# Kernel optimization log

Measured on AMD Instinct MI355X. Metric: run time of the kernel, lower is better.

Reference implementation:

```python
import jax, jax.numpy as jnp
import numpy as np

NHEAD = 16


def setup_inputs() -> dict:
    key = jax.random.key(0)
    ks = jax.random.split(key, 6)
    S, B, D = 2048, 2, 1024
    std = float(np.sqrt(6.0 / (D + D)))  # xavier_uniform bound
    inp = {
        "query": jax.random.normal(ks[0], (S, B, D), jnp.float32),
        "key": jax.random.normal(ks[1], (S, B, D), jnp.float32),
        "value": jax.random.normal(ks[2], (S, B, D), jnp.float32),
        "Wq": jax.random.uniform(ks[3], (D, D), jnp.float32, -std, std),
        "bq": jnp.ones((D,), jnp.float32),
        "Wk": jax.random.uniform(ks[4], (D, D), jnp.float32, -std, std),
        "bk": jnp.ones((D,), jnp.float32),
        "Wv": jax.random.uniform(ks[5], (D, D), jnp.float32, -std, std),
        "bv": jnp.ones((D,), jnp.float32),
    }
    return inp


def reference(query, key, value, Wq, bq, Wk, bk, Wv, bv):
    S, B, D = query.shape
    h = NHEAD
    d = D // h
    scale = jnp.asarray(d ** 0.5, query.dtype)
    # projections (nn.Linear: x @ W^T + b)
    q = (query @ Wq.T + bq).reshape(S, B, h, d)
    k = (key @ Wk.T + bk).reshape(S, B, h, d)
    v = (value @ Wv.T + bv).reshape(S, B, h, d)
    # batch_first=False path: scores [b,h,i,j], softmax over j, then AV
    scores = jnp.einsum('ibhd,jbhd->bhij', q, k) / scale
    attn = jax.nn.softmax(scores, axis=-1)
    out = jnp.einsum('bhij,jbhd->ibhd', attn, v).reshape(S, B, D)
    return out
```

## Files before the change

kernel.cpp:

```cpp
#include <hip/hip_runtime.h>
#include <hip/hip_bf16.h>

#define S_LEN 2048
#define BATCH 2
#define DMODEL 1024
#define NHEAD 16
#define HDIM 64
#define MTOT (S_LEN * BATCH)
#define QKV_ELEMS ((size_t)MTOT * DMODEL)

typedef __bf16 bf16x8 __attribute__((ext_vector_type(8)));
typedef unsigned short u16x8 __attribute__((ext_vector_type(8)));
typedef float f32x4 __attribute__((ext_vector_type(4)));
typedef float f32x16 __attribute__((ext_vector_type(16)));
typedef unsigned int u32x4 __attribute__((ext_vector_type(4)));

__device__ __forceinline__ unsigned short f2bf(float f) {
    unsigned int u = __float_as_uint(f);
    u += 0x7FFFu + ((u >> 16) & 1u);
    return (unsigned short)(u >> 16);
}

#define PBM 128
#define PBN 128
#define PBK 32
#define PLDS 48
#define QSCALE 0.18033688011112042f

__global__ __launch_bounds__(256) void proj_kernel(
        const float* __restrict__ Xq, const float* __restrict__ Xk,
        const float* __restrict__ Xv, const float* __restrict__ Wq,
        const float* __restrict__ Wk, const float* __restrict__ Wv,
        const float* __restrict__ bq, const float* __restrict__ bk,
        const float* __restrict__ bv, unsigned short* __restrict__ ws)
{
    const int t = blockIdx.z;
    const float* X    = (t == 0) ? Xq : (t == 1) ? Xk : Xv;
    const float* W    = (t == 0) ? Wq : (t == 1) ? Wk : Wv;
    const float* bias = (t == 0) ? bq : (t == 1) ? bk : bv;
    unsigned short* out = ws + (size_t)t * QKV_ELEMS;
    const float scale = (t == 0) ? QSCALE : 1.0f;

    __shared__ __align__(16) unsigned short lds[(PBM + PBN) * PLDS];
    unsigned short* Alds = lds;
    unsigned short* Blds = lds + PBM * PLDS;

    const int tid = threadIdx.x;
    const int m0 = blockIdx.y * PBM;
    const int n0 = blockIdx.x * PBN;

    const int wave = tid >> 6;
    const int lane = tid & 63;
    const int lrow = lane & 15;
    const int lg   = lane >> 4;
    const int wr = (wave >> 1) * 64;
    const int wc = (wave & 1) * 64;

    f32x4 acc[4][4];
#pragma unroll
    for (int i = 0; i < 4; ++i)
#pragma unroll
        for (int j = 0; j < 4; ++j)
            acc[i][j] = (f32x4){0.f, 0.f, 0.f, 0.f};

    const int sr = tid >> 3;
    const int sg = tid & 7;

    for (int k0 = 0; k0 < DMODEL; k0 += PBK) {
        __syncthreads();
#pragma unroll
        for (int it = 0; it < 4; ++it) {
            const int row = sr + it * 32;
            const float4 va = *(const float4*)(X + (size_t)(m0 + row) * DMODEL + k0 + sg * 4);
            const float4 vb = *(const float4*)(W + (size_t)(n0 + row) * DMODEL + k0 + sg * 4);
            ushort4 ha, hb;
            ha.x = f2bf(va.x); ha.y = f2bf(va.y); ha.z = f2bf(va.z); ha.w = f2bf(va.w);
            hb.x = f2bf(vb.x); hb.y = f2bf(vb.y); hb.z = f2bf(vb.z); hb.w = f2bf(vb.w);
            *(ushort4*)&Alds[row * PLDS + sg * 4] = ha;
            *(ushort4*)&Blds[row * PLDS + sg * 4] = hb;
        }
        __syncthreads();

        bf16x8 af[4], bw[4];
#pragma unroll
        for (int i = 0; i < 4; ++i) {
            af[i] = *(const bf16x8*)&Alds[(wr + i * 16 + lrow) * PLDS + lg * 8];
            bw[i] = *(const bf16x8*)&Blds[(wc + i * 16 + lrow) * PLDS + lg * 8];
        }
#pragma unroll
        for (int i = 0; i < 4; ++i)
#pragma unroll
            for (int j = 0; j < 4; ++j)
                acc[i][j] = __builtin_amdgcn_mfma_f32_16x16x32_bf16(af[i], bw[j], acc[i][j], 0, 0, 0);
    }

#pragma unroll
    for (int j = 0; j < 4; ++j) {
        const int n  = n0 + wc + j * 16 + lrow;
        const float bv_ = bias[n];
        const int h  = n >> 6;
        const int dd = n & 63;
#pragma unroll
        for (int i = 0; i < 4; ++i) {
#pragma unroll
            for (int r = 0; r < 4; ++r) {
                const int m = m0 + wr + i * 16 + lg * 4 + r;
                const int s = m >> 1;
                const int b = m & 1;
                const float v = (acc[i][j][r] + bv_) * scale;
                size_t idx;
                if (t == 2)
                    idx = ((size_t)((b * NHEAD + h) * HDIM + dd)) * S_LEN + s;
                else
                    idx = ((size_t)((b * NHEAD + h) * S_LEN + s)) * HDIM + dd;
                out[idx] = f2bf(v);
            }
        }
    }
}

__global__ __launch_bounds__(512) void attn_kernel(
        const unsigned short* __restrict__ ws, float* __restrict__ out)
{
    const unsigned short* Qw = ws;
    const unsigned short* Kw = ws + QKV_ELEMS;
    const unsigned short* Vw = ws + 2 * QKV_ELEMS;

    const int bid = blockIdx.x;
    const int idx = bid >> 3;
    const int bh  = (bid & 7) * 4 + (idx >> 3);
    const int q0  = (idx & 7) * 256;

    __shared__ __align__(16) unsigned short Klds[64 * 64];
    __shared__ __align__(16) unsigned short Vlds[64 * 64];
    __shared__ unsigned int Pu[8][32 * 32];

    const int tid  = threadIdx.x;
    const int wave = tid >> 6;
    const int lane = tid & 63;
    const int l31  = lane & 31;
    const int half = lane >> 5;

    const size_t base = (size_t)bh * S_LEN * HDIM;
    const int qrow = q0 + wave * 32 + l31;

    bf16x8 qf[4];
#pragma unroll
    for (int c = 0; c < 4; ++c)
        qf[c] = *(const bf16x8*)(Qw + base + (size_t)qrow * HDIM + c * 16 + half * 8);

    f32x16 Od0, Od1;
#pragma unroll
    for (int i = 0; i < 16; ++i) { Od0[i] = 0.f; Od1[i] = 0.f; }
    float mrun = -__builtin_inff();
    float lrun = 0.f;

    const int srow = tid >> 3;
    const int sg   = tid & 7;

    for (int s0 = 0; s0 < S_LEN; s0 += 64) {
        __syncthreads();
        {
            const int gsw = (sg ^ (srow & 7)) * 8;
            *(u16x8*)&Klds[srow * 64 + gsw] =
                *(const u16x8*)(Kw + base + (size_t)(s0 + srow) * HDIM + sg * 8);
            *(u16x8*)&Vlds[srow * 64 + gsw] =
                *(const u16x8*)(Vw + base + (size_t)srow * S_LEN + s0 + sg * 8);
        }
        __syncthreads();

        f32x16 S0, S1;
#pragma unroll
        for (int i = 0; i < 16; ++i) { S0[i] = 0.f; S1[i] = 0.f; }
#pragma unroll
        for (int c = 0; c < 4; ++c) {
            const int g = ((c * 2 + half) ^ (l31 & 7)) * 8;
            const bf16x8 ka0 = *(const bf16x8*)&Klds[l31 * 64 + g];
            const bf16x8 ka1 = *(const bf16x8*)&Klds[(32 + l31) * 64 + g];
            S0 = __builtin_amdgcn_mfma_f32_32x32x16_bf16(ka0, qf[c], S0, 0, 0, 0);
            S1 = __builtin_amdgcn_mfma_f32_32x32x16_bf16(ka1, qf[c], S1, 0, 0, 0);
        }

        float mx = S0[0];
#pragma unroll
        for (int i = 1; i < 16; ++i) mx = fmaxf(mx, S0[i]);
#pragma unroll
        for (int i = 0; i < 16; ++i) mx = fmaxf(mx, S1[i]);
        mx = fmaxf(mx, __shfl_xor(mx, 32, 64));

        const float mnew = fmaxf(mrun, mx);
        const float ex   = exp2f(mrun - mnew);
        mrun = mnew;

        float psum = 0.f;
#pragma unroll
        for (int i = 0; i < 16; ++i) { S0[i] = exp2f(S0[i] - mnew); psum += S0[i]; }
#pragma unroll
        for (int i = 0; i < 16; ++i) { S1[i] = exp2f(S1[i] - mnew); psum += S1[i]; }
        psum += __shfl_xor(psum, 32, 64);
        lrun = lrun * ex + psum;
        Od0 *= ex;
        Od1 *= ex;

#pragma unroll
        for (int w = 0; w < 8; ++w) {
            const unsigned int pk0 = (unsigned int)f2bf(S0[2 * w])
                                   | ((unsigned int)f2bf(S0[2 * w + 1]) << 16);
            const unsigned int pk1 = (unsigned int)f2bf(S1[2 * w])
                                   | ((unsigned int)f2bf(S1[2 * w + 1]) << 16);
            const int kp = (w & 1) + 4 * (w >> 1) + 2 * half;
            Pu[wave][kp * 32 + l31]        = pk0;
            Pu[wave][(16 + kp) * 32 + l31] = pk1;
        }
        __asm__ volatile("" ::: "memory");

#pragma unroll
        for (int c = 0; c < 4; ++c) {
            const int g = ((c * 2 + half) ^ (l31 & 7)) * 8;
            const bf16x8 va0 = *(const bf16x8*)&Vlds[l31 * 64 + g];
            const bf16x8 va1 = *(const bf16x8*)&Vlds[(32 + l31) * 64 + g];
            u32x4 pu;
#pragma unroll
            for (int e = 0; e < 4; ++e)
                pu[e] = Pu[wave][(c * 8 + half * 4 + e) * 32 + l31];
            const bf16x8 pb = __builtin_bit_cast(bf16x8, pu);
            Od0 = __builtin_amdgcn_mfma_f32_32x32x16_bf16(va0, pb, Od0, 0, 0, 0);
            Od1 = __builtin_amdgcn_mfma_f32_32x32x16_bf16(va1, pb, Od1, 0, 0, 0);
        }
    }

    const int bb = bh >> 4;
    const int hh = bh & 15;
    const float inv = 1.0f / lrun;
    float* op = out + (size_t)qrow * (BATCH * DMODEL) + bb * DMODEL + hh * HDIM;
#pragma unroll
    for (int gg = 0; gg < 4; ++gg) {
        const int d0 = gg * 8 + half * 4;
        float4 v0, v1;
        v0.x = Od0[gg * 4 + 0] * inv; v0.y = Od0[gg * 4 + 1] * inv;
        v0.z = Od0[gg * 4 + 2] * inv; v0.w = Od0[gg * 4 + 3] * inv;
        v1.x = Od1[gg * 4 + 0] * inv; v1.y = Od1[gg * 4 + 1] * inv;
        v1.z = Od1[gg * 4 + 2] * inv; v1.w = Od1[gg * 4 + 3] * inv;
        *(float4*)(op + d0)      = v0;
        *(float4*)(op + 32 + d0) = v1;
    }
}

extern "C" void kernel_launch(void* const* d_in, const int* in_sizes, int n_in,
                              void* d_out, int out_size, void* d_ws, size_t ws_size,
                              hipStream_t stream) {
    const float* q  = (const float*)d_in[0];
    const float* k  = (const float*)d_in[1];
    const float* v  = (const float*)d_in[2];
    const float* Wq = (const float*)d_in[3];
    const float* bq = (const float*)d_in[4];
    const float* Wk = (const float*)d_in[5];
    const float* bk = (const float*)d_in[6];
    const float* Wv = (const float*)d_in[7];
    const float* bv = (const float*)d_in[8];
    unsigned short* ws = (unsigned short*)d_ws;
    float* out = (float*)d_out;

    dim3 pgrid(DMODEL / PBN, MTOT / PBM, 3);
    proj_kernel<<<pgrid, dim3(256), 0, stream>>>(q, k, v, Wq, Wk, Wv, bq, bk, bv, ws);

    attn_kernel<<<dim3(256), dim3(512), 0, stream>>>(ws, out);
}
```

Baseline: 157.7 us.

## Double-buffer K/V tiles via direct global-to-LDS loads with lazy softmax rescale

The attention kernel now prefetches the next K/V tile into a second LDS buffer using direct global-to-LDS loads while computing the current tile. This removes one barrier per iteration and aims to hide global load latency. Blocks shrink to 4 waves with 128 query rows, and the grid doubles to 512 blocks for more parallelism. Online-softmax rescaling is skipped unless the running max grows by more than 8 (in log2 units), MFMA sections are wrapped in s_setprio, and the max and sum reductions become trees. The lazy rescale trades exact max tracking for fewer multiplies, bounded by the threshold.

Result: no change. 160.9 us (+2.0%).

```diff
diff --git a/kernel.cpp b/kernel.cpp
--- a/kernel.cpp
+++ b/kernel.cpp
@@ -19,6 +19,12 @@
     unsigned int u = __float_as_uint(f);
     u += 0x7FFFu + ((u >> 16) & 1u);
     return (unsigned short)(u >> 16);
+}
+
+__device__ __forceinline__ void gload_lds16(const void* g, void* l) {
+    __builtin_amdgcn_global_load_lds(
+        (const __attribute__((address_space(1))) unsigned int*)g,
+        (__attribute__((address_space(3))) unsigned int*)l, 16, 0, 0);
 }
 
 #define PBM 128
@@ -119,7 +125,9 @@
     }
 }
 
-__global__ __launch_bounds__(512) void attn_kernel(
+#define NT (S_LEN / 64)
+
+__global__ __launch_bounds__(256) void attn_kernel(
         const unsigned short* __restrict__ ws, float* __restrict__ out)
 {
     const unsigned short* Qw = ws;
@@ -128,12 +136,12 @@
 
     const int bid = blockIdx.x;
     const int idx = bid >> 3;
-    const int bh  = (bid & 7) * 4 + (idx >> 3);
-    const int q0  = (idx & 7) * 256;
-
-    __shared__ __align__(16) unsigned short Klds[64 * 64];
-    __shared__ __align__(16) unsigned short Vlds[64 * 64];
-    __shared__ unsigned int Pu[8][32 * 32];
+    const int bh  = (bid & 7) * 4 + (idx >> 4);
+    const int q0  = (idx & 15) * 128;
+
+    __shared__ __align__(16) unsigned short Kbuf[2][64 * 64];
+    __shared__ __align__(16) unsigned short Vbuf[2][64 * 64];
+    __shared__ unsigned int Pu[4][32 * 32];
 
     const int tid  = threadIdx.x;
     const int wave = tid >> 6;
@@ -155,23 +163,34 @@
     float mrun = -__builtin_inff();
     float lrun = 0.f;
 
-    const int srow = tid >> 3;
-    const int sg   = tid & 7;
-
-    for (int s0 = 0; s0 < S_LEN; s0 += 64) {
-        __syncthreads();
-        {
-            const int gsw = (sg ^ (srow & 7)) * 8;
-            *(u16x8*)&Klds[srow * 64 + gsw] =
-                *(const u16x8*)(Kw + base + (size_t)(s0 + srow) * HDIM + sg * 8);
-            *(u16x8*)&Vlds[srow * 64 + gsw] =
-                *(const u16x8*)(Vw + base + (size_t)srow * S_LEN + s0 + sg * 8);
-        }
-        __syncthreads();
+    const int strow = lane >> 3;
+    const int sgrp  = (lane & 7) ^ strow;
+    const int r0    = wave * 16 + strow;
+    const int dstoff = wave * 1024 + lane * 8;
+
+    gload_lds16(Kw + base + (size_t)r0 * HDIM + sgrp * 8,        &Kbuf[0][dstoff]);
+    gload_lds16(Kw + base + (size_t)(r0 + 8) * HDIM + sgrp * 8,  &Kbuf[0][dstoff + 512]);
+    gload_lds16(Vw + base + (size_t)r0 * S_LEN + sgrp * 8,       &Vbuf[0][dstoff]);
+    gload_lds16(Vw + base + (size_t)(r0 + 8) * S_LEN + sgrp * 8, &Vbuf[0][dstoff + 512]);
+    __syncthreads();
+
+    int cur = 0;
+    for (int t = 0; t < NT; ++t) {
+        if (t + 1 < NT) {
+            const int sn = (t + 1) * 64;
+            gload_lds16(Kw + base + (size_t)(sn + r0) * HDIM + sgrp * 8,       &Kbuf[cur ^ 1][dstoff]);
+            gload_lds16(Kw + base + (size_t)(sn + r0 + 8) * HDIM + sgrp * 8,   &Kbuf[cur ^ 1][dstoff + 512]);
+            gload_lds16(Vw + base + (size_t)r0 * S_LEN + sn + sgrp * 8,        &Vbuf[cur ^ 1][dstoff]);
+            gload_lds16(Vw + base + (size_t)(r0 + 8) * S_LEN + sn + sgrp * 8,  &Vbuf[cur ^ 1][dstoff + 512]);
+        }
+
+        const unsigned short* Klds = Kbuf[cur];
+        const unsigned short* Vlds = Vbuf[cur];
 
         f32x16 S0, S1;
 #pragma unroll
         for (int i = 0; i < 16; ++i) { S0[i] = 0.f; S1[i] = 0.f; }
+        __builtin_amdgcn_s_setprio(1);
 #pragma unroll
         for (int c = 0; c < 4; ++c) {
             const int g = ((c * 2 + half) ^ (l31 & 7)) * 8;
@@ -180,27 +199,42 @@
             S0 = __builtin_amdgcn_mfma_f32_32x32x16_bf16(ka0, qf[c], S0, 0, 0, 0);
             S1 = __builtin_amdgcn_mfma_f32_32x32x16_bf16(ka1, qf[c], S1, 0, 0, 0);
         }
-
-        float mx = S0[0];
-#pragma unroll
-        for (int i = 1; i < 16; ++i) mx = fmaxf(mx, S0[i]);
-#pragma unroll
-        for (int i = 0; i < 16; ++i) mx = fmaxf(mx, S1[i]);
+        __builtin_amdgcn_s_setprio(0);
+
+        f32x16 mx16;
+#pragma unroll
+        for (int i = 0; i < 16; ++i) mx16[i] = fmaxf(S0[i], S1[i]);
+        float m8[8], m4[4], m2[2];
+#pragma unroll
+        for (int i = 0; i < 8; ++i) m8[i] = fmaxf(mx16[i], mx16[i + 8]);
+#pragma unroll
+        for (int i = 0; i < 4; ++i) m4[i] = fmaxf(m8[i], m8[i + 4]);
+        m2[0] = fmaxf(m4[0], m4[2]); m2[1] = fmaxf(m4[1], m4[3]);
+        float mx = fmaxf(m2[0], m2[1]);
         mx = fmaxf(mx, __shfl_xor(mx, 32, 64));
 
-        const float mnew = fmaxf(mrun, mx);
-        const float ex   = exp2f(mrun - mnew);
-        mrun = mnew;
-
-        float psum = 0.f;
-#pragma unroll
-        for (int i = 0; i < 16; ++i) { S0[i] = exp2f(S0[i] - mnew); psum += S0[i]; }
-#pragma unroll
-        for (int i = 0; i < 16; ++i) { S1[i] = exp2f(S1[i] - mnew); psum += S1[i]; }
+        if (!__all(mx - mrun <= 8.0f)) {
+            const float mnew = fmaxf(mrun, mx);
+            const float ex   = exp2f(mrun - mnew);
+            mrun = mnew;
+            lrun *= ex;
+            Od0 *= ex;
+            Od1 *= ex;
+        }
+
+#pragma unroll
+        for (int i = 0; i < 16; ++i) S0[i] = exp2f(S0[i] - mrun);
+#pragma unroll
+        for (int i = 0; i < 16; ++i) S1[i] = exp2f(S1[i] - mrun);
+        f32x16 sv = S0 + S1;
+        float s8[8], s4[4];
+#pragma unroll
+        for (int i = 0; i < 8; ++i) s8[i] = sv[i] + sv[i + 8];
+#pragma unroll
+        for (int i = 0; i < 4; ++i) s4[i] = s8[i] + s8[i + 4];
+        float psum = (s4[0] + s4[2]) + (s4[1] + s4[3]);
         psum += __shfl_xor(psum, 32, 64);
-        lrun = lrun * ex + psum;
-        Od0 *= ex;
-        Od1 *= ex;
+        lrun += psum;
 
 #pragma unroll
         for (int w = 0; w < 8; ++w) {
@@ -214,6 +248,7 @@
         }
         __asm__ volatile("" ::: "memory");
 
+        __builtin_amdgcn_s_setprio(1);
 #pragma unroll
         for (int c = 0; c < 4; ++c) {
             const int g = ((c * 2 + half) ^ (l31 & 7)) * 8;
@@ -227,6 +262,10 @@
             Od0 = __builtin_amdgcn_mfma_f32_32x32x16_bf16(va0, pb, Od0, 0, 0, 0);
             Od1 = __builtin_amdgcn_mfma_f32_32x32x16_bf16(va1, pb, Od1, 0, 0, 0);
         }
+        __builtin_amdgcn_s_setprio(0);
+
+        __syncthreads();
+        cur ^= 1;
     }
 
     const int bb = bh >> 4;
@@ -264,5 +303,5 @@
     dim3 pgrid(DMODEL / PBN, MTOT / PBM, 3);
     proj_kernel<<<pgrid, dim3(256), 0, stream>>>(q, k, v, Wq, Wk, Wv, bq, bk, bv, ws);
 
-    attn_kernel<<<dim3(256), dim3(512), 0, stream>>>(ws, out);
-}
+    attn_kernel<<<dim3(512), dim3(256), 0, stream>>>(ws, out);
+}
```
